# Performance work log

Measured on AMD Instinct MI355X. Metric: run time of the kernel, lower is better.

Reference implementation:

```python
import jax, jax.numpy as jnp
import numpy as np

TEMPERATURE = 8.0


def setup_inputs() -> dict:
    key = jax.random.key(0)
    kq, kk, kv, km = jax.random.split(key, 4)
    B, H, S, D = 2, 16, 2048, 64
    q = jax.random.normal(kq, (B, H, S, D), dtype=jnp.float32)
    k = jax.random.normal(kk, (B, H, S, D), dtype=jnp.float32)
    v = jax.random.normal(kv, (B, H, S, D), dtype=jnp.float32)
    mask = jax.random.randint(km, (B, S, S), 0, 2, dtype=jnp.int32)
    return {"q": q, "k": k, "v": v, "mask": mask}


def reference(q, k, v, mask):
    # attn = q @ k^T / temperature  -> [B,H,Sq,Sk]
    attn = jnp.einsum("bhqd,bhkd->bhqk", q, k) / TEMPERATURE
    # mask: [B,Sq,Sk] -> [B,1,Sq,Sk]; masked where mask == 0
    m0 = (mask == 0)[:, None, :, :]
    attn = jnp.where(m0, -jnp.inf, attn)
    attn = jax.nn.softmax(attn, axis=-1)
    attn = jnp.where(m0, 0.0, attn)
    output = jnp.einsum("bhqk,bhkd->bhqd", attn, v)
    return (output, attn)
```

## Files before the change

### kernel.cpp

```cpp
#include <hip/hip_runtime.h>


#define S 2048
#define D 64
#define HH 16
#define BB 2
#define LDK 72
#define PSTR 36

typedef __attribute__((ext_vector_type(8))) short short8;
typedef __attribute__((ext_vector_type(4))) float f32x4;

__device__ __forceinline__ unsigned int f2bfu(float f) {
  unsigned int u = __builtin_bit_cast(unsigned int, f);
  u += 0x7fffu + ((u >> 16) & 1u);
  return u >> 16;
}
__device__ __forceinline__ unsigned int packbf2(float a, float b) {
  return f2bfu(a) | (f2bfu(b) << 16);
}
__device__ __forceinline__ short8 cvt8(float4 a, float4 b) {
  union { unsigned int u[4]; short8 s; } r;
  r.u[0] = packbf2(a.x, a.y); r.u[1] = packbf2(a.z, a.w);
  r.u[2] = packbf2(b.x, b.y); r.u[3] = packbf2(b.z, b.w);
  return r.s;
}

__global__ __launch_bounds__(256) void pack_mask_kernel(
    const int* __restrict__ m, unsigned long long* __restrict__ bits) {
  int wid = blockIdx.x * 4 + (threadIdx.x >> 6);
  int lane = threadIdx.x & 63;
  int v = m[(size_t)wid * 64 + lane];
  unsigned long long b = __ballot(v != 0);
  if (lane == 0) bits[wid] = b;
}

__global__ __launch_bounds__(256) void attn_kernel(
    const float* __restrict__ Qg, const float* __restrict__ Kg,
    const float* __restrict__ Vg, const unsigned long long* __restrict__ Mb,
    float* __restrict__ Og, float* __restrict__ Ag) {
  __shared__ unsigned short Kt[64 * LDK];
  __shared__ unsigned short Vt[64 * LDK];
  __shared__ unsigned int Pp[4 * 16 * PSTR];

  const int tid = threadIdx.x;
  const int w = tid >> 6;
  const int lane = tid & 63;
  const int ln15 = lane & 15;
  const int quad = lane >> 4;

  const int bh = blockIdx.x;
  const int qtile = blockIdx.y;
  const int b = bh >> 4;
  const size_t qkvbase = (size_t)bh * S * D;
  const int q0 = qtile * 64;
  const int qrow = q0 + w * 16 + ln15;

  const float4* qp = reinterpret_cast<const float4*>(Qg + qkvbase + (size_t)qrow * D);
  short8 aq0, aq1;
  {
    float4 a0 = qp[quad * 2], a1 = qp[quad * 2 + 1];
    float4 b0 = qp[8 + quad * 2], b1 = qp[8 + quad * 2 + 1];
    aq0 = cvt8(a0, a1);
    aq1 = cvt8(b0, b1);
  }

  const unsigned long long* mrow = Mb + ((size_t)b * S + qrow) * (S / 64);

  const int trow = tid >> 2;
  const int tcol = (tid & 3) << 4;

  float lsum = 0.f;
  float4 kf0, kf1, kf2, kf3;
  {
    const float4* src = reinterpret_cast<const float4*>(Kg + qkvbase + (size_t)trow * D + tcol);
    kf0 = src[0]; kf1 = src[1]; kf2 = src[2]; kf3 = src[3];
  }
  unsigned long long mw = mrow[0];
  for (int t = 0; t < 32; ++t) {
    __syncthreads();
    *reinterpret_cast<short8*>(&Kt[trow * LDK + tcol]) = cvt8(kf0, kf1);
    *reinterpret_cast<short8*>(&Kt[trow * LDK + tcol + 8]) = cvt8(kf2, kf3);
    __syncthreads();
    if (t < 31) {
      const float4* src = reinterpret_cast<const float4*>(
          Kg + qkvbase + (size_t)((t + 1) * 64 + trow) * D + tcol);
      kf0 = src[0]; kf1 = src[1]; kf2 = src[2]; kf3 = src[3];
    }
    unsigned long long mwn = (t < 31) ? mrow[t + 1] : 0ULL;
#pragma unroll
    for (int kt = 0; kt < 4; ++kt) {
      short8 bk0 = *reinterpret_cast<const short8*>(&Kt[(kt * 16 + ln15) * LDK + (quad << 3)]);
      short8 bk1 = *reinterpret_cast<const short8*>(&Kt[(kt * 16 + ln15) * LDK + 32 + (quad << 3)]);
      f32x4 acc = {0.f, 0.f, 0.f, 0.f};
      acc = __builtin_amdgcn_mfma_f32_16x16x32_bf16(bk0, aq0, acc, 0, 0, 0);
      acc = __builtin_amdgcn_mfma_f32_16x16x32_bf16(bk1, aq1, acc, 0, 0, 0);
      unsigned int nib = (unsigned int)(mw >> (kt * 16 + quad * 4)) & 0xFu;
#pragma unroll
      for (int r = 0; r < 4; ++r) {
        float e = __expf(acc[r] * 0.125f);
        lsum += ((nib >> r) & 1u) ? e : 0.f;
      }
    }
    mw = mwn;
  }
  lsum += __shfl_xor(lsum, 16, 64);
  lsum += __shfl_xor(lsum, 32, 64);
  const float rinv = (lsum > 0.f) ? 1.f / lsum : 0.f;

  float* arow = Ag + ((size_t)bh * S + qrow) * S;
  f32x4 oacc[4] = {{0.f, 0.f, 0.f, 0.f}, {0.f, 0.f, 0.f, 0.f},
                   {0.f, 0.f, 0.f, 0.f}, {0.f, 0.f, 0.f, 0.f}};
  unsigned int* Pw = Pp + w * 16 * PSTR;

  float4 vf0, vf1, vf2, vf3;
  {
    const float4* src = reinterpret_cast<const float4*>(Kg + qkvbase + (size_t)trow * D + tcol);
    kf0 = src[0]; kf1 = src[1]; kf2 = src[2]; kf3 = src[3];
    const float4* vs = reinterpret_cast<const float4*>(Vg + qkvbase + (size_t)trow * D + tcol);
    vf0 = vs[0]; vf1 = vs[1]; vf2 = vs[2]; vf3 = vs[3];
  }
  mw = mrow[0];
  for (int t = 0; t < 32; ++t) {
    __syncthreads();
    *reinterpret_cast<short8*>(&Kt[trow * LDK + tcol]) = cvt8(kf0, kf1);
    *reinterpret_cast<short8*>(&Kt[trow * LDK + tcol + 8]) = cvt8(kf2, kf3);
    {
      float yy[16] = {vf0.x, vf0.y, vf0.z, vf0.w, vf1.x, vf1.y, vf1.z, vf1.w,
                      vf2.x, vf2.y, vf2.z, vf2.w, vf3.x, vf3.y, vf3.z, vf3.w};
#pragma unroll
      for (int j = 0; j < 16; ++j) {
        int d = tcol + j;
        int pg = (trow >> 3) ^ ((d >> 3) & 7);
        Vt[d * LDK + pg * 8 + (trow & 7)] = (unsigned short)f2bfu(yy[j]);
      }
    }
    __syncthreads();
    if (t < 31) {
      const float4* src = reinterpret_cast<const float4*>(
          Kg + qkvbase + (size_t)((t + 1) * 64 + trow) * D + tcol);
      kf0 = src[0]; kf1 = src[1]; kf2 = src[2]; kf3 = src[3];
      const float4* vs = reinterpret_cast<const float4*>(
          Vg + qkvbase + (size_t)((t + 1) * 64 + trow) * D + tcol);
      vf0 = vs[0]; vf1 = vs[1]; vf2 = vs[2]; vf3 = vs[3];
    }
    unsigned long long mwn = (t < 31) ? mrow[t + 1] : 0ULL;
    const int k0 = t * 64;
#pragma unroll
    for (int kt = 0; kt < 4; ++kt) {
      short8 bk0 = *reinterpret_cast<const short8*>(&Kt[(kt * 16 + ln15) * LDK + (quad << 3)]);
      short8 bk1 = *reinterpret_cast<const short8*>(&Kt[(kt * 16 + ln15) * LDK + 32 + (quad << 3)]);
      f32x4 acc = {0.f, 0.f, 0.f, 0.f};
      acc = __builtin_amdgcn_mfma_f32_16x16x32_bf16(bk0, aq0, acc, 0, 0, 0);
      acc = __builtin_amdgcn_mfma_f32_16x16x32_bf16(bk1, aq1, acc, 0, 0, 0);
      unsigned int nib = (unsigned int)(mw >> (kt * 16 + quad * 4)) & 0xFu;
      f32x4 p;
#pragma unroll
      for (int r = 0; r < 4; ++r) {
        float e = __expf(acc[r] * 0.125f) * rinv;
        p[r] = ((nib >> r) & 1u) ? e : 0.f;
      }
      *reinterpret_cast<f32x4*>(arow + k0 + kt * 16 + quad * 4) = p;
      Pw[ln15 * PSTR + kt * 8 + quad * 2] = packbf2(p[0], p[1]);
      Pw[ln15 * PSTR + kt * 8 + quad * 2 + 1] = packbf2(p[2], p[3]);
    }
#pragma unroll
    for (int kc = 0; kc < 2; ++kc) {
      short8 ap = *reinterpret_cast<const short8*>(&Pw[ln15 * PSTR + kc * 16 + quad * 4]);
#pragma unroll
      for (int c = 0; c < 4; ++c) {
        int dr = c * 16 + ln15;
        int pg = (4 * kc + quad) ^ ((dr >> 3) & 7);
        short8 bv = *reinterpret_cast<const short8*>(&Vt[dr * LDK + pg * 8]);
        oacc[c] = __builtin_amdgcn_mfma_f32_16x16x32_bf16(ap, bv, oacc[c], 0, 0, 0);
      }
    }
    mw = mwn;
  }

#pragma unroll
  for (int c = 0; c < 4; ++c) {
#pragma unroll
    for (int r = 0; r < 4; ++r) {
      Og[qkvbase + (size_t)(q0 + w * 16 + quad * 4 + r) * D + c * 16 + ln15] = oacc[c][r];
    }
  }
}

extern "C" void kernel_launch(void* const* d_in, const int* in_sizes, int n_in,
                              void* d_out, int out_size, void* d_ws, size_t ws_size,
                              hipStream_t stream) {
  const float* q = (const float*)d_in[0];
  const float* k = (const float*)d_in[1];
  const float* v = (const float*)d_in[2];
  const int* m = (const int*)d_in[3];
  float* outp = (float*)d_out;
  float* attnp = outp + (size_t)BB * HH * S * D;
  unsigned long long* bits = (unsigned long long*)d_ws;

  const int nwords = BB * S * (S / 64);
  pack_mask_kernel<<<nwords / 4, 256, 0, stream>>>(m, bits);
  dim3 grid(BB * HH, S / 64);
  attn_kernel<<<grid, 256, 0, stream>>>(q, k, v, bits, outp, attnp);
}
```

Baseline: 804.2 us.

## Use transposing LDS reads for V, keep P in registers, fold scale into Q

Stores V to shared memory in its natural row-major layout and reads it back with ds_read_b64_tr_b16 transposing loads. This replaces the scattered per-element transposed scalar stores. The probability tile is kept in registers as MFMA A-operands instead of being round-tripped through a shared P buffer. The 1/8 temperature is folded into Q before the bf16 conversion, bf16 conversion uses the native cast, and the attention matrix is written with nontemporal stores. The inline asm and manual waitcnt depend on a specific fragment mapping and constrain compiler scheduling.

```diff
diff --git a/kernel.cpp b/kernel.cpp
--- a/kernel.cpp
+++ b/kernel.cpp
@@ -6,18 +6,16 @@
 #define HH 16
 #define BB 2
 #define LDK 72
-#define PSTR 36
 
 typedef __attribute__((ext_vector_type(8))) short short8;
 typedef __attribute__((ext_vector_type(4))) float f32x4;
-
-__device__ __forceinline__ unsigned int f2bfu(float f) {
-  unsigned int u = __builtin_bit_cast(unsigned int, f);
-  u += 0x7fffu + ((u >> 16) & 1u);
-  return u >> 16;
-}
+typedef __attribute__((ext_vector_type(2))) unsigned int u32x2;
+
 __device__ __forceinline__ unsigned int packbf2(float a, float b) {
-  return f2bfu(a) | (f2bfu(b) << 16);
+  union { __bf16 h[2]; unsigned int u; } r;
+  r.h[0] = (__bf16)a;
+  r.h[1] = (__bf16)b;
+  return r.u;
 }
 __device__ __forceinline__ short8 cvt8(float4 a, float4 b) {
   union { unsigned int u[4]; short8 s; } r;
@@ -25,6 +23,12 @@
   r.u[2] = packbf2(b.x, b.y); r.u[3] = packbf2(b.z, b.w);
   return r.s;
 }
+__device__ __forceinline__ float4 qscale(float4 v) {
+  return make_float4(v.x * 0.125f, v.y * 0.125f, v.z * 0.125f, v.w * 0.125f);
+}
+
+#define TRRD(dst, addr, off) \
+  asm volatile("ds_read_b64_tr_b16 %0, %1 offset:" #off : "=v"(dst) : "v"(addr))
 
 __global__ __launch_bounds__(256) void pack_mask_kernel(
     const int* __restrict__ m, unsigned long long* __restrict__ bits) {
@@ -39,9 +43,8 @@
     const float* __restrict__ Qg, const float* __restrict__ Kg,
     const float* __restrict__ Vg, const unsigned long long* __restrict__ Mb,
     float* __restrict__ Og, float* __restrict__ Ag) {
+  __shared__ alignas(128) unsigned short Vt[64 * 64];
   __shared__ unsigned short Kt[64 * LDK];
-  __shared__ unsigned short Vt[64 * LDK];
-  __shared__ unsigned int Pp[4 * 16 * PSTR];
 
   const int tid = threadIdx.x;
   const int w = tid >> 6;
@@ -59,8 +62,8 @@
   const float4* qp = reinterpret_cast<const float4*>(Qg + qkvbase + (size_t)qrow * D);
   short8 aq0, aq1;
   {
-    float4 a0 = qp[quad * 2], a1 = qp[quad * 2 + 1];
-    float4 b0 = qp[8 + quad * 2], b1 = qp[8 + quad * 2 + 1];
+    float4 a0 = qscale(qp[quad * 2]), a1 = qscale(qp[quad * 2 + 1]);
+    float4 b0 = qscale(qp[8 + quad * 2]), b1 = qscale(qp[8 + quad * 2 + 1]);
     aq0 = cvt8(a0, a1);
     aq1 = cvt8(b0, b1);
   }
@@ -98,7 +101,7 @@
       unsigned int nib = (unsigned int)(mw >> (kt * 16 + quad * 4)) & 0xFu;
 #pragma unroll
       for (int r = 0; r < 4; ++r) {
-        float e = __expf(acc[r] * 0.125f);
+        float e = __expf(acc[r]);
         lsum += ((nib >> r) & 1u) ? e : 0.f;
       }
     }
@@ -111,7 +114,10 @@
   float* arow = Ag + ((size_t)bh * S + qrow) * S;
   f32x4 oacc[4] = {{0.f, 0.f, 0.f, 0.f}, {0.f, 0.f, 0.f, 0.f},
                    {0.f, 0.f, 0.f, 0.f}, {0.f, 0.f, 0.f, 0.f}};
-  unsigned int* Pw = Pp + w * 16 * PSTR;
+
+  const unsigned int vbase = (unsigned int)(unsigned long long)(const void*)&Vt[0];
+  const unsigned int vb = vbase + (unsigned int)(quad * 512 + ln15 * 8);
+  const int vwoff = ((trow >> 2) * 4 + (tid & 3)) * 64 + (trow & 3) * 16;
 
   float4 vf0, vf1, vf2, vf3;
   {
@@ -125,16 +131,8 @@
     __syncthreads();
     *reinterpret_cast<short8*>(&Kt[trow * LDK + tcol]) = cvt8(kf0, kf1);
     *reinterpret_cast<short8*>(&Kt[trow * LDK + tcol + 8]) = cvt8(kf2, kf3);
-    {
-      float yy[16] = {vf0.x, vf0.y, vf0.z, vf0.w, vf1.x, vf1.y, vf1.z, vf1.w,
-                      vf2.x, vf2.y, vf2.z, vf2.w, vf3.x, vf3.y, vf3.z, vf3.w};
-#pragma unroll
-      for (int j = 0; j < 16; ++j) {
-        int d = tcol + j;
-        int pg = (trow >> 3) ^ ((d >> 3) & 7);
-        Vt[d * LDK + pg * 8 + (trow & 7)] = (unsigned short)f2bfu(yy[j]);
-      }
-    }
+    *reinterpret_cast<short8*>(&Vt[vwoff]) = cvt8(vf0, vf1);
+    *reinterpret_cast<short8*>(&Vt[vwoff + 8]) = cvt8(vf2, vf3);
     __syncthreads();
     if (t < 31) {
       const float4* src = reinterpret_cast<const float4*>(
@@ -146,6 +144,7 @@
     }
     unsigned long long mwn = (t < 31) ? mrow[t + 1] : 0ULL;
     const int k0 = t * 64;
+    unsigned int apu[8];
 #pragma unroll
     for (int kt = 0; kt < 4; ++kt) {
       short8 bk0 = *reinterpret_cast<const short8*>(&Kt[(kt * 16 + ln15) * LDK + (quad << 3)]);
@@ -157,24 +156,44 @@
       f32x4 p;
 #pragma unroll
       for (int r = 0; r < 4; ++r) {
-        float e = __expf(acc[r] * 0.125f) * rinv;
+        float e = __expf(acc[r]) * rinv;
         p[r] = ((nib >> r) & 1u) ? e : 0.f;
       }
-      *reinterpret_cast<f32x4*>(arow + k0 + kt * 16 + quad * 4) = p;
-      Pw[ln15 * PSTR + kt * 8 + quad * 2] = packbf2(p[0], p[1]);
-      Pw[ln15 * PSTR + kt * 8 + quad * 2 + 1] = packbf2(p[2], p[3]);
-    }
-#pragma unroll
-    for (int kc = 0; kc < 2; ++kc) {
-      short8 ap = *reinterpret_cast<const short8*>(&Pw[ln15 * PSTR + kc * 16 + quad * 4]);
-#pragma unroll
-      for (int c = 0; c < 4; ++c) {
-        int dr = c * 16 + ln15;
-        int pg = (4 * kc + quad) ^ ((dr >> 3) & 7);
-        short8 bv = *reinterpret_cast<const short8*>(&Vt[dr * LDK + pg * 8]);
-        oacc[c] = __builtin_amdgcn_mfma_f32_16x16x32_bf16(ap, bv, oacc[c], 0, 0, 0);
-      }
-    }
+      __builtin_nontemporal_store(p, reinterpret_cast<f32x4*>(arow + k0 + kt * 16 + quad * 4));
+      apu[kt * 2] = packbf2(p[0], p[1]);
+      apu[kt * 2 + 1] = packbf2(p[2], p[3]);
+    }
+    u32x2 x0, x1, x2, x3, x4, x5, x6, x7, x8, x9, x10, x11, x12, x13, x14, x15;
+    TRRD(x0, vb, 0);     TRRD(x1, vb, 2048);
+    TRRD(x2, vb, 128);   TRRD(x3, vb, 2176);
+    TRRD(x4, vb, 256);   TRRD(x5, vb, 2304);
+    TRRD(x6, vb, 384);   TRRD(x7, vb, 2432);
+    TRRD(x8, vb, 4096);  TRRD(x9, vb, 6144);
+    TRRD(x10, vb, 4224); TRRD(x11, vb, 6272);
+    TRRD(x12, vb, 4352); TRRD(x13, vb, 6400);
+    TRRD(x14, vb, 4480); TRRD(x15, vb, 6528);
+    asm volatile("s_waitcnt lgkmcnt(0)" ::: "memory");
+    __builtin_amdgcn_sched_barrier(0);
+    union Frag { unsigned int u[4]; u32x2 d[2]; short8 s; };
+    Frag ap0, ap1, bv;
+    ap0.u[0] = apu[0]; ap0.u[1] = apu[1]; ap0.u[2] = apu[2]; ap0.u[3] = apu[3];
+    ap1.u[0] = apu[4]; ap1.u[1] = apu[5]; ap1.u[2] = apu[6]; ap1.u[3] = apu[7];
+    bv.d[0] = x0;  bv.d[1] = x1;
+    oacc[0] = __builtin_amdgcn_mfma_f32_16x16x32_bf16(ap0.s, bv.s, oacc[0], 0, 0, 0);
+    bv.d[0] = x2;  bv.d[1] = x3;
+    oacc[1] = __builtin_amdgcn_mfma_f32_16x16x32_bf16(ap0.s, bv.s, oacc[1], 0, 0, 0);
+    bv.d[0] = x4;  bv.d[1] = x5;
+    oacc[2] = __builtin_amdgcn_mfma_f32_16x16x32_bf16(ap0.s, bv.s, oacc[2], 0, 0, 0);
+    bv.d[0] = x6;  bv.d[1] = x7;
+    oacc[3] = __builtin_amdgcn_mfma_f32_16x16x32_bf16(ap0.s, bv.s, oacc[3], 0, 0, 0);
+    bv.d[0] = x8;  bv.d[1] = x9;
+    oacc[0] = __builtin_amdgcn_mfma_f32_16x16x32_bf16(ap1.s, bv.s, oacc[0], 0, 0, 0);
+    bv.d[0] = x10; bv.d[1] = x11;
+    oacc[1] = __builtin_amdgcn_mfma_f32_16x16x32_bf16(ap1.s, bv.s, oacc[1], 0, 0, 0);
+    bv.d[0] = x12; bv.d[1] = x13;
+    oacc[2] = __builtin_amdgcn_mfma_f32_16x16x32_bf16(ap1.s, bv.s, oacc[2], 0, 0, 0);
+    bv.d[0] = x14; bv.d[1] = x15;
+    oacc[3] = __builtin_amdgcn_mfma_f32_16x16x32_bf16(ap1.s, bv.s, oacc[3], 0, 0, 0);
     mw = mwn;
   }
 
```

Measured after the change: 795.5 us. No clear change (-1.1%).
